# Kernel optimization log

Hardware: AMD Instinct MI355X
Metric: run time of the kernel (lower is better)

The kernel has to match this reference:

```python
import jax, jax.numpy as jnp
import numpy as np

# dipy lower-triangular channel order: [Dxx, Dxy, Dyy, Dxz, Dyz, Dzz]
_LOTRI_IDX = np.array([[0, 1, 3], [1, 2, 4], [3, 4, 5]])


def _trilinear_warp(img, ddf):
    """MONAI Warp(mode='bilinear', padding_mode='border'): sample img at voxel
    coords (index + ddf), trilinear interp, clamped to borders.
    img: (B,C,H,W,D), ddf: (B,3,H,W,D) in voxel units."""
    B, C, H, W, D = img.shape
    f = img.dtype
    gx, gy, gz = jnp.meshgrid(jnp.arange(H, dtype=f), jnp.arange(W, dtype=f),
                              jnp.arange(D, dtype=f), indexing='ij')
    cx = jnp.clip(gx[None] + ddf[:, 0], 0.0, H - 1.0)
    cy = jnp.clip(gy[None] + ddf[:, 1], 0.0, W - 1.0)
    cz = jnp.clip(gz[None] + ddf[:, 2], 0.0, D - 1.0)
    x0f = jnp.floor(cx); y0f = jnp.floor(cy); z0f = jnp.floor(cz)
    fx = (cx - x0f)[:, None]; fy = (cy - y0f)[:, None]; fz = (cz - z0f)[:, None]
    x0 = x0f.astype(jnp.int32); y0 = y0f.astype(jnp.int32); z0 = z0f.astype(jnp.int32)
    x1 = jnp.minimum(x0 + 1, H - 1); y1 = jnp.minimum(y0 + 1, W - 1); z1 = jnp.minimum(z0 + 1, D - 1)
    flat = img.reshape(B, C, H * W * D)

    def g(ix, iy, iz):
        lin = (ix * W + iy) * D + iz  # (B,H,W,D)
        return jnp.take_along_axis(flat, lin.reshape(B, 1, -1), axis=2).reshape(B, C, H, W, D)

    c00 = g(x0, y0, z0) * (1 - fz) + g(x0, y0, z1) * fz
    c01 = g(x0, y1, z0) * (1 - fz) + g(x0, y1, z1) * fz
    c10 = g(x1, y0, z0) * (1 - fz) + g(x1, y0, z1) * fz
    c11 = g(x1, y1, z0) * (1 - fz) + g(x1, y1, z1) * fz
    c0 = c00 * (1 - fy) + c01 * fy
    c1 = c10 * (1 - fy) + c11 * fy
    return c0 * (1 - fx) + c1 * fx


def _jacobian(ddf):
    """J = I + d(ddf)/dx via central differences (one-sided at edges).
    Returns (B,H,W,D,3,3) with J[...,i,j] = delta_ij + d ddf_i / d x_j."""
    rows = [jnp.stack(jnp.gradient(ddf[:, i], axis=(1, 2, 3)), axis=-1) for i in range(3)]
    J = jnp.stack(rows, axis=-2)  # (B,H,W,D,3,3)
    return J + jnp.eye(3, dtype=ddf.dtype)


def _forward(dti, ddf):
    warped = _trilinear_warp(dti, ddf)                    # (B,6,H,W,D)
    wc = jnp.moveaxis(warped, 1, -1)                      # (B,H,W,D,6)
    M = wc[..., jnp.asarray(_LOTRI_IDX)]                  # (B,H,W,D,3,3) symmetric
    J = _jacobian(ddf)
    U, _, Vh = jnp.linalg.svd(J, full_matrices=False)
    R = U @ Vh                                            # polar orthogonal factor
    Dp = jnp.einsum('...ji,...jk,...kl->...il', R, M, R)  # R^T M R
    lot = jnp.stack([Dp[..., 0, 0], Dp[..., 1, 0], Dp[..., 1, 1],
                     Dp[..., 2, 0], Dp[..., 2, 1], Dp[..., 2, 2]], axis=1)
    return lot


def setup_inputs() -> dict:
    key = jax.random.key(0)
    k1, k2 = jax.random.split(key)
    B, H, W, D = 1, 128, 128, 128
    dti = jax.random.normal(k1, (B, 6, H, W, D), dtype=jnp.float32)
    ddf = jax.random.normal(k2, (B, 3, H, W, D), dtype=jnp.float32)
    return {"dti": dti, "ddf": ddf}


def reference(dti, ddf):
    return _forward(dti, ddf)
```

## Files before the change

### kernel.cpp

```cpp
#include <hip/hip_runtime.h>
#include <hip/hip_fp16.h>
#include <math.h>

#define DIM 128
#define NVOX (DIM*DIM*DIM)

__global__ __launch_bounds__(256) void pack_dti_kernel(
    const float* __restrict__ dti, uint4* __restrict__ aos)
{
    const int id = blockIdx.x * 256 + threadIdx.x;
    const __half2 h01 = __floats2half2_rn(dti[0 * NVOX + id], dti[1 * NVOX + id]);
    const __half2 h23 = __floats2half2_rn(dti[2 * NVOX + id], dti[3 * NVOX + id]);
    const __half2 h45 = __floats2half2_rn(dti[4 * NVOX + id], dti[5 * NVOX + id]);
    uint4 q;
    q.x = *reinterpret_cast<const unsigned int*>(&h01);
    q.y = *reinterpret_cast<const unsigned int*>(&h23);
    q.z = *reinterpret_cast<const unsigned int*>(&h45);
    q.w = 0u;
    aos[id] = q;
}

__device__ __forceinline__ bool polar_f32(const float J[9], float X[9])
{
#pragma unroll
    for (int t = 0; t < 9; ++t) X[t] = J[t];
    bool bad = false;
#pragma unroll
    for (int it = 0; it < 7; ++it) {
        float C[9];
        C[0] = X[4] * X[8] - X[5] * X[7];
        C[1] = X[5] * X[6] - X[3] * X[8];
        C[2] = X[3] * X[7] - X[4] * X[6];
        C[3] = X[2] * X[7] - X[1] * X[8];
        C[4] = X[0] * X[8] - X[2] * X[6];
        C[5] = X[1] * X[6] - X[0] * X[7];
        C[6] = X[1] * X[5] - X[2] * X[4];
        C[7] = X[2] * X[3] - X[0] * X[5];
        C[8] = X[0] * X[4] - X[1] * X[3];
        const float det = X[0] * C[0] + X[1] * C[1] + X[2] * C[2];
        float a, b;
        if (it < 3) {
            float nX = 0.0f, nC = 0.0f;
#pragma unroll
            for (int t = 0; t < 9; ++t) { nX += X[t] * X[t]; nC += C[t] * C[t]; }
            if (it == 0)
                bad = !(__builtin_amdgcn_sqrtf(nX * nC) < 2.0e3f * fabsf(det));
            const float s = __builtin_amdgcn_sqrtf(nC * __builtin_amdgcn_rcpf(nX));
            const float g = __builtin_amdgcn_sqrtf(s * __builtin_amdgcn_rcpf(fabsf(det)));
            a = 0.5f * g;
            b = copysignf(0.5f * g * __builtin_amdgcn_rcpf(s), det);
        } else {
            a = 0.5f;
            b = 0.5f * __builtin_amdgcn_rcpf(det);
        }
#pragma unroll
        for (int t = 0; t < 9; ++t) X[t] = a * X[t] + b * C[t];
    }
    return bad;
}

__device__ __forceinline__ void polar_f64(const float J[9], float X[9])
{
    double Y[9];
#pragma unroll
    for (int t = 0; t < 9; ++t) Y[t] = (double)J[t];
    for (int it = 0; it < 20; ++it) {
        double C[9];
        C[0] = Y[4] * Y[8] - Y[5] * Y[7];
        C[1] = Y[5] * Y[6] - Y[3] * Y[8];
        C[2] = Y[3] * Y[7] - Y[4] * Y[6];
        C[3] = Y[2] * Y[7] - Y[1] * Y[8];
        C[4] = Y[0] * Y[8] - Y[2] * Y[6];
        C[5] = Y[1] * Y[6] - Y[0] * Y[7];
        C[6] = Y[1] * Y[5] - Y[2] * Y[4];
        C[7] = Y[2] * Y[3] - Y[0] * Y[5];
        C[8] = Y[0] * Y[4] - Y[1] * Y[3];
        const double det = Y[0] * C[0] + Y[1] * C[1] + Y[2] * C[2];
        if (!(fabs(det) > 1e-300)) break;
        double nX = 0.0, nC = 0.0;
#pragma unroll
        for (int t = 0; t < 9; ++t) { nX += Y[t] * Y[t]; nC += C[t] * C[t]; }
        const double g = sqrt(sqrt(nC) / (fabs(det) * sqrt(nX)));
        const double a = 0.5 * g;
        const double b = 0.5 / (g * det);
        double diff2 = 0.0, n2 = 0.0;
#pragma unroll
        for (int t = 0; t < 9; ++t) {
            const double y = a * Y[t] + b * C[t];
            const double d = y - Y[t];
            diff2 += d * d; n2 += y * y;
            Y[t] = y;
        }
        if (diff2 <= 1e-26 * n2) break;
    }
#pragma unroll
    for (int t = 0; t < 9; ++t) X[t] = (float)Y[t];
}

__global__ __launch_bounds__(256) void warp_dti_kernel(
    const uint4* __restrict__ aos,
    const float* __restrict__ ddf,
    float* __restrict__ out)
{
    const int id = blockIdx.x * 256 + threadIdx.x;
    const int k = id & (DIM - 1);
    const int j = (id >> 7) & (DIM - 1);
    const int i = id >> 14;

    const int im = (i > 0) ? i - 1 : 0, ip = (i < DIM - 1) ? i + 1 : DIM - 1;
    const int jm = (j > 0) ? j - 1 : 0, jp = (j < DIM - 1) ? j + 1 : DIM - 1;
    const int km = (k > 0) ? k - 1 : 0, kp = (k < DIM - 1) ? k + 1 : DIM - 1;
    const float si = (ip - im == 2) ? 0.5f : 1.0f;
    const float sj = (jp - jm == 2) ? 0.5f : 1.0f;
    const float sk = (kp - km == 2) ? 0.5f : 1.0f;

    const int l_ip = (ip << 14) | (j << 7) | k;
    const int l_im = (im << 14) | (j << 7) | k;
    const int l_jp = (i << 14) | (jp << 7) | k;
    const int l_jm = (i << 14) | (jm << 7) | k;
    const int l_kp = (i << 14) | (j << 7) | kp;
    const int l_km = (i << 14) | (j << 7) | km;

    float J[9];
    float u[3];
#pragma unroll
    for (int c = 0; c < 3; ++c) {
        const float* __restrict__ p = ddf + c * NVOX;
        u[c] = p[id];
        J[c * 3 + 0] = (p[l_ip] - p[l_im]) * si;
        J[c * 3 + 1] = (p[l_jp] - p[l_jm]) * sj;
        J[c * 3 + 2] = (p[l_kp] - p[l_km]) * sk;
        J[c * 3 + c] += 1.0f;
    }

    const float cx = fminf(fmaxf((float)i + u[0], 0.0f), (float)(DIM - 1));
    const float cy = fminf(fmaxf((float)j + u[1], 0.0f), (float)(DIM - 1));
    const float cz = fminf(fmaxf((float)k + u[2], 0.0f), (float)(DIM - 1));
    const float x0f = floorf(cx), y0f = floorf(cy), z0f = floorf(cz);
    const float fx = cx - x0f, fy = cy - y0f, fz = cz - z0f;
    const int x0 = (int)x0f, y0 = (int)y0f, z0 = (int)z0f;
    const int x1 = min(x0 + 1, DIM - 1);
    const int y1 = min(y0 + 1, DIM - 1);
    const int z1 = min(z0 + 1, DIM - 1);

    const float gx0 = 1.0f - fx, gy0 = 1.0f - fy, gz0 = 1.0f - fz;

    float acc0 = 0.0f, acc1 = 0.0f, acc2 = 0.0f;
    float acc3 = 0.0f, acc4 = 0.0f, acc5 = 0.0f;

    auto gat = [&](int lin, float wt) {
        const uint4 q = aos[lin];
        const float2 f01 = __half22float2(*reinterpret_cast<const __half2*>(&q.x));
        const float2 f23 = __half22float2(*reinterpret_cast<const __half2*>(&q.y));
        const float2 f45 = __half22float2(*reinterpret_cast<const __half2*>(&q.z));
        acc0 = fmaf(wt, f01.x, acc0);
        acc1 = fmaf(wt, f01.y, acc1);
        acc2 = fmaf(wt, f23.x, acc2);
        acc3 = fmaf(wt, f23.y, acc3);
        acc4 = fmaf(wt, f45.x, acc4);
        acc5 = fmaf(wt, f45.y, acc5);
    };

    gat((x0 << 14) | (y0 << 7) | z0, gx0 * gy0 * gz0);
    gat((x0 << 14) | (y0 << 7) | z1, gx0 * gy0 * fz);
    gat((x0 << 14) | (y1 << 7) | z0, gx0 * fy * gz0);
    gat((x0 << 14) | (y1 << 7) | z1, gx0 * fy * fz);
    gat((x1 << 14) | (y0 << 7) | z0, fx * gy0 * gz0);
    gat((x1 << 14) | (y0 << 7) | z1, fx * gy0 * fz);
    gat((x1 << 14) | (y1 << 7) | z0, fx * fy * gz0);
    gat((x1 << 14) | (y1 << 7) | z1, fx * fy * fz);

    float X[9];
    const bool bad = polar_f32(J, X);
    if (__builtin_expect(bad, 0)) polar_f64(J, X);

    const float M00 = acc0, M01 = acc1, M11 = acc2;
    const float M02 = acc3, M12 = acc4, M22 = acc5;
    float P[9];
    P[0] = M00 * X[0] + M01 * X[3] + M02 * X[6];
    P[1] = M00 * X[1] + M01 * X[4] + M02 * X[7];
    P[2] = M00 * X[2] + M01 * X[5] + M02 * X[8];
    P[3] = M01 * X[0] + M11 * X[3] + M12 * X[6];
    P[4] = M01 * X[1] + M11 * X[4] + M12 * X[7];
    P[5] = M01 * X[2] + M11 * X[5] + M12 * X[8];
    P[6] = M02 * X[0] + M12 * X[3] + M22 * X[6];
    P[7] = M02 * X[1] + M12 * X[4] + M22 * X[7];
    P[8] = M02 * X[2] + M12 * X[5] + M22 * X[8];

    out[0 * NVOX + id] = X[0] * P[0] + X[3] * P[3] + X[6] * P[6];
    out[1 * NVOX + id] = X[1] * P[0] + X[4] * P[3] + X[7] * P[6];
    out[2 * NVOX + id] = X[1] * P[1] + X[4] * P[4] + X[7] * P[7];
    out[3 * NVOX + id] = X[2] * P[0] + X[5] * P[3] + X[8] * P[6];
    out[4 * NVOX + id] = X[2] * P[1] + X[5] * P[4] + X[8] * P[7];
    out[5 * NVOX + id] = X[2] * P[2] + X[5] * P[5] + X[8] * P[8];
}

extern "C" void kernel_launch(void* const* d_in, const int* in_sizes, int n_in,
                              void* d_out, int out_size, void* d_ws, size_t ws_size,
                              hipStream_t stream) {
    const float* dti = (const float*)d_in[0];
    const float* ddf = (const float*)d_in[1];
    float* out = (float*)d_out;
    uint4* aos = (uint4*)d_ws;

    const int nblk = NVOX / 256;
    hipLaunchKernelGGL(pack_dti_kernel, dim3(nblk), dim3(256), 0, stream,
                       dti, aos);
    hipLaunchKernelGGL(warp_dti_kernel, dim3(nblk), dim3(256), 0, stream,
                       aos, ddf, out);
}
```

Baseline: 169.6 us.

## Vectorize DTI packing, swizzle block order, trim polar iterations, nontemporal I/O

The pack kernel now handles four voxels per thread using 128-bit nontemporal loads. Both kernels remap block indices in an XCD-style interleave so that neighbouring data lands on the same die. The polar iteration drops from 7 to 6 steps, replaces two sqrt and reciprocal ops with a single rsq, and computes the 8 gather addresses from offsets added to one base. Output stores are nontemporal. The changes aim to cut memory traffic cost and ALU work, at some risk to accuracy from the shorter polar iteration.

```diff
diff --git a/kernel.cpp b/kernel.cpp
--- a/kernel.cpp
+++ b/kernel.cpp
@@ -5,19 +5,39 @@
 #define DIM 128
 #define NVOX (DIM*DIM*DIM)
 
+typedef float vfloat4 __attribute__((ext_vector_type(4)));
+typedef unsigned int vuint4 __attribute__((ext_vector_type(4)));
+
 __global__ __launch_bounds__(256) void pack_dti_kernel(
-    const float* __restrict__ dti, uint4* __restrict__ aos)
-{
-    const int id = blockIdx.x * 256 + threadIdx.x;
-    const __half2 h01 = __floats2half2_rn(dti[0 * NVOX + id], dti[1 * NVOX + id]);
-    const __half2 h23 = __floats2half2_rn(dti[2 * NVOX + id], dti[3 * NVOX + id]);
-    const __half2 h45 = __floats2half2_rn(dti[4 * NVOX + id], dti[5 * NVOX + id]);
-    uint4 q;
-    q.x = *reinterpret_cast<const unsigned int*>(&h01);
-    q.y = *reinterpret_cast<const unsigned int*>(&h23);
-    q.z = *reinterpret_cast<const unsigned int*>(&h45);
-    q.w = 0u;
-    aos[id] = q;
+    const float* __restrict__ dti, vuint4* __restrict__ aos)
+{
+    const int bid = blockIdx.x;
+    const int sb = ((bid & 7) << 8) | (bid >> 3);
+    const int id4 = (sb * 256 + (int)threadIdx.x) * 4;
+
+    const vfloat4 v0 = __builtin_nontemporal_load(reinterpret_cast<const vfloat4*>(dti + 0 * NVOX + id4));
+    const vfloat4 v1 = __builtin_nontemporal_load(reinterpret_cast<const vfloat4*>(dti + 1 * NVOX + id4));
+    const vfloat4 v2 = __builtin_nontemporal_load(reinterpret_cast<const vfloat4*>(dti + 2 * NVOX + id4));
+    const vfloat4 v3 = __builtin_nontemporal_load(reinterpret_cast<const vfloat4*>(dti + 3 * NVOX + id4));
+    const vfloat4 v4 = __builtin_nontemporal_load(reinterpret_cast<const vfloat4*>(dti + 4 * NVOX + id4));
+    const vfloat4 v5 = __builtin_nontemporal_load(reinterpret_cast<const vfloat4*>(dti + 5 * NVOX + id4));
+
+    auto packone = [&](float a0, float a1, float a2, float a3, float a4,
+                       float a5, int idx) {
+        const __half2 h01 = __floats2half2_rn(a0, a1);
+        const __half2 h23 = __floats2half2_rn(a2, a3);
+        const __half2 h45 = __floats2half2_rn(a4, a5);
+        vuint4 q;
+        q.x = *reinterpret_cast<const unsigned int*>(&h01);
+        q.y = *reinterpret_cast<const unsigned int*>(&h23);
+        q.z = *reinterpret_cast<const unsigned int*>(&h45);
+        q.w = 0u;
+        aos[idx] = q;
+    };
+    packone(v0.x, v1.x, v2.x, v3.x, v4.x, v5.x, id4 + 0);
+    packone(v0.y, v1.y, v2.y, v3.y, v4.y, v5.y, id4 + 1);
+    packone(v0.z, v1.z, v2.z, v3.z, v4.z, v5.z, id4 + 2);
+    packone(v0.w, v1.w, v2.w, v3.w, v4.w, v5.w, id4 + 3);
 }
 
 __device__ __forceinline__ bool polar_f32(const float J[9], float X[9])
@@ -26,7 +46,7 @@
     for (int t = 0; t < 9; ++t) X[t] = J[t];
     bool bad = false;
 #pragma unroll
-    for (int it = 0; it < 7; ++it) {
+    for (int it = 0; it < 6; ++it) {
         float C[9];
         C[0] = X[4] * X[8] - X[5] * X[7];
         C[1] = X[5] * X[6] - X[3] * X[8];
@@ -44,11 +64,11 @@
 #pragma unroll
             for (int t = 0; t < 9; ++t) { nX += X[t] * X[t]; nC += C[t] * C[t]; }
             if (it == 0)
-                bad = !(__builtin_amdgcn_sqrtf(nX * nC) < 2.0e3f * fabsf(det));
+                bad = !(nX * nC < 4.0e6f * det * det);
             const float s = __builtin_amdgcn_sqrtf(nC * __builtin_amdgcn_rcpf(nX));
-            const float g = __builtin_amdgcn_sqrtf(s * __builtin_amdgcn_rcpf(fabsf(det)));
-            a = 0.5f * g;
-            b = copysignf(0.5f * g * __builtin_amdgcn_rcpf(s), det);
+            const float r = __builtin_amdgcn_rsqf(s * fabsf(det));
+            a = 0.5f * s * r;
+            b = copysignf(0.5f * r, det);
         } else {
             a = 0.5f;
             b = 0.5f * __builtin_amdgcn_rcpf(det);
@@ -98,11 +118,13 @@
 }
 
 __global__ __launch_bounds__(256) void warp_dti_kernel(
-    const uint4* __restrict__ aos,
+    const vuint4* __restrict__ aos,
     const float* __restrict__ ddf,
     float* __restrict__ out)
 {
-    const int id = blockIdx.x * 256 + threadIdx.x;
+    const int bid = blockIdx.x;
+    const int sb = ((bid & 7) << 10) | (bid >> 3);
+    const int id = sb * 256 + (int)threadIdx.x;
     const int k = id & (DIM - 1);
     const int j = (id >> 7) & (DIM - 1);
     const int i = id >> 14;
@@ -145,30 +167,36 @@
 
     const float gx0 = 1.0f - fx, gy0 = 1.0f - fy, gz0 = 1.0f - fz;
 
+    const int dz = z1 - z0;
+    const int dy = (y1 - y0) << 7;
+    const int dx = (x1 - x0) << 14;
+    const int b000 = (x0 << 14) | (y0 << 7) | z0;
+
     float acc0 = 0.0f, acc1 = 0.0f, acc2 = 0.0f;
     float acc3 = 0.0f, acc4 = 0.0f, acc5 = 0.0f;
 
     auto gat = [&](int lin, float wt) {
-        const uint4 q = aos[lin];
-        const float2 f01 = __half22float2(*reinterpret_cast<const __half2*>(&q.x));
-        const float2 f23 = __half22float2(*reinterpret_cast<const __half2*>(&q.y));
-        const float2 f45 = __half22float2(*reinterpret_cast<const __half2*>(&q.z));
-        acc0 = fmaf(wt, f01.x, acc0);
-        acc1 = fmaf(wt, f01.y, acc1);
-        acc2 = fmaf(wt, f23.x, acc2);
-        acc3 = fmaf(wt, f23.y, acc3);
-        acc4 = fmaf(wt, f45.x, acc4);
-        acc5 = fmaf(wt, f45.y, acc5);
+        const vuint4 q = aos[lin];
+        const unsigned int qx = q.x, qy = q.y, qz = q.z;
+        const __half2 h01 = *reinterpret_cast<const __half2*>(&qx);
+        const __half2 h23 = *reinterpret_cast<const __half2*>(&qy);
+        const __half2 h45 = *reinterpret_cast<const __half2*>(&qz);
+        acc0 = fmaf(__half2float(__low2half(h01)), wt, acc0);
+        acc1 = fmaf(__half2float(__high2half(h01)), wt, acc1);
+        acc2 = fmaf(__half2float(__low2half(h23)), wt, acc2);
+        acc3 = fmaf(__half2float(__high2half(h23)), wt, acc3);
+        acc4 = fmaf(__half2float(__low2half(h45)), wt, acc4);
+        acc5 = fmaf(__half2float(__high2half(h45)), wt, acc5);
     };
 
-    gat((x0 << 14) | (y0 << 7) | z0, gx0 * gy0 * gz0);
-    gat((x0 << 14) | (y0 << 7) | z1, gx0 * gy0 * fz);
-    gat((x0 << 14) | (y1 << 7) | z0, gx0 * fy * gz0);
-    gat((x0 << 14) | (y1 << 7) | z1, gx0 * fy * fz);
-    gat((x1 << 14) | (y0 << 7) | z0, fx * gy0 * gz0);
-    gat((x1 << 14) | (y0 << 7) | z1, fx * gy0 * fz);
-    gat((x1 << 14) | (y1 << 7) | z0, fx * fy * gz0);
-    gat((x1 << 14) | (y1 << 7) | z1, fx * fy * fz);
+    gat(b000,                gx0 * gy0 * gz0);
+    gat(b000 + dz,           gx0 * gy0 * fz);
+    gat(b000 + dy,           gx0 * fy * gz0);
+    gat(b000 + dy + dz,      gx0 * fy * fz);
+    gat(b000 + dx,           fx * gy0 * gz0);
+    gat(b000 + dx + dz,      fx * gy0 * fz);
+    gat(b000 + dx + dy,      fx * fy * gz0);
+    gat(b000 + dx + dy + dz, fx * fy * fz);
 
     float X[9];
     const bool bad = polar_f32(J, X);
@@ -187,12 +215,12 @@
     P[7] = M02 * X[1] + M12 * X[4] + M22 * X[7];
     P[8] = M02 * X[2] + M12 * X[5] + M22 * X[8];
 
-    out[0 * NVOX + id] = X[0] * P[0] + X[3] * P[3] + X[6] * P[6];
-    out[1 * NVOX + id] = X[1] * P[0] + X[4] * P[3] + X[7] * P[6];
-    out[2 * NVOX + id] = X[1] * P[1] + X[4] * P[4] + X[7] * P[7];
-    out[3 * NVOX + id] = X[2] * P[0] + X[5] * P[3] + X[8] * P[6];
-    out[4 * NVOX + id] = X[2] * P[1] + X[5] * P[4] + X[8] * P[7];
-    out[5 * NVOX + id] = X[2] * P[2] + X[5] * P[5] + X[8] * P[8];
+    __builtin_nontemporal_store(X[0] * P[0] + X[3] * P[3] + X[6] * P[6], &out[0 * NVOX + id]);
+    __builtin_nontemporal_store(X[1] * P[0] + X[4] * P[3] + X[7] * P[6], &out[1 * NVOX + id]);
+    __builtin_nontemporal_store(X[1] * P[1] + X[4] * P[4] + X[7] * P[7], &out[2 * NVOX + id]);
+    __builtin_nontemporal_store(X[2] * P[0] + X[5] * P[3] + X[8] * P[6], &out[3 * NVOX + id]);
+    __builtin_nontemporal_store(X[2] * P[1] + X[5] * P[4] + X[8] * P[7], &out[4 * NVOX + id]);
+    __builtin_nontemporal_store(X[2] * P[2] + X[5] * P[5] + X[8] * P[8], &out[5 * NVOX + id]);
 }
 
 extern "C" void kernel_launch(void* const* d_in, const int* in_sizes, int n_in,
@@ -201,11 +229,10 @@
     const float* dti = (const float*)d_in[0];
     const float* ddf = (const float*)d_in[1];
     float* out = (float*)d_out;
-    uint4* aos = (uint4*)d_ws;
-
-    const int nblk = NVOX / 256;
-    hipLaunchKernelGGL(pack_dti_kernel, dim3(nblk), dim3(256), 0, stream,
+    vuint4* aos = (vuint4*)d_ws;
+
+    hipLaunchKernelGGL(pack_dti_kernel, dim3(NVOX / 1024), dim3(256), 0, stream,
                        dti, aos);
-    hipLaunchKernelGGL(warp_dti_kernel, dim3(nblk), dim3(256), 0, stream,
+    hipLaunchKernelGGL(warp_dti_kernel, dim3(NVOX / 256), dim3(256), 0, stream,
                        aos, ddf, out);
 }
```

Result: no change. 169.0 us (-0.4%).
